# Kernel tuning notes

Measured on AMD Instinct MI355X. Metric: run time of the kernel, lower is better.

## Reference

```python
import jax, jax.numpy as jnp
import numpy as np

N_NODES = 50000
N_EDGES = 640000
HIDDEN = 128
EDGE_FEATS = 16
NUM_LAYERS = 4
NUM_GRAPHS = 64
LN_EPS = 1e-5


def setup_inputs() -> dict:
    key = jax.random.key(0)
    ks = jax.random.split(key, 12)
    s = 1.0 / np.sqrt(HIDDEN)
    se = 1.0 / np.sqrt(EDGE_FEATS)
    return {
        "x": jax.random.normal(ks[0], (N_NODES, HIDDEN), jnp.float32),
        "batch_index": jnp.sort(jax.random.randint(ks[1], (N_NODES,), 0, NUM_GRAPHS)),
        "edge_index": jax.random.randint(ks[2], (2, N_EDGES), 0, N_NODES),
        "edge_attr": jax.random.normal(ks[3], (N_EDGES, EDGE_FEATS), jnp.float32),
        # edge_transform Linear(EDGE_FEATS -> HIDDEN)
        "We": jax.random.uniform(ks[4], (EDGE_FEATS, HIDDEN), jnp.float32, -se, se),
        "be": jax.random.uniform(ks[5], (HIDDEN,), jnp.float32, -se, se),
        # per-layer GINE MLP: Linear-ReLU-Linear, stacked over layers
        "W1": jax.random.uniform(ks[6], (NUM_LAYERS, HIDDEN, HIDDEN), jnp.float32, -s, s),
        "b1": jax.random.uniform(ks[7], (NUM_LAYERS, HIDDEN), jnp.float32, -s, s),
        "W2": jax.random.uniform(ks[8], (NUM_LAYERS, HIDDEN, HIDDEN), jnp.float32, -s, s),
        "b2": jax.random.uniform(ks[9], (NUM_LAYERS, HIDDEN), jnp.float32, -s, s),
        # per-layer LayerNorm params
        "ln_g": jnp.ones((NUM_LAYERS, HIDDEN), jnp.float32),
        "ln_b": jnp.zeros((NUM_LAYERS, HIDDEN), jnp.float32),
    }


def reference(x, batch_index, edge_index, edge_attr, We, be, W1, b1, W2, b2, ln_g, ln_b):
    n = x.shape[0]
    src, dst = edge_index[0], edge_index[1]
    ea = edge_attr @ We + be  # [E, H] shared across layers
    h = x
    for l in range(W1.shape[0]):
        # GINEConv message: ReLU(x_j + edge_attr), scatter-sum at dst
        m = jax.nn.relu(h[src] + ea)
        agg = jax.ops.segment_sum(m, dst, num_segments=n)
        z = h + agg  # (1 + eps) * x + agg with eps = 0
        z = jax.nn.relu(z @ W1[l] + b1[l]) @ W2[l] + b2[l]
        # LayerNorm over feature dim
        mu = jnp.mean(z, axis=-1, keepdims=True)
        var = jnp.var(z, axis=-1, keepdims=True)
        z = (z - mu) / jnp.sqrt(var + LN_EPS) * ln_g[l] + ln_b[l]
        # dropout(p=0) is identity
        h = jax.nn.relu(z) + h
    return h
```

## Files before the change

kernel.cpp:

```cpp
#include <hip/hip_runtime.h>

#define HIDDEN 128
#define NLAYERS 4

typedef __attribute__((ext_vector_type(8))) short short8;
typedef __attribute__((ext_vector_type(4))) float f32x4;

__device__ __forceinline__ ushort f2bf(float f) {
    uint x = __builtin_bit_cast(uint, f);
    return (ushort)((x + 0x7fffu + ((x >> 16) & 1u)) >> 16);
}
__device__ __forceinline__ float bflo(uint u) {
    return __builtin_bit_cast(float, u << 16);
}
__device__ __forceinline__ float bfhi(uint u) {
    return __builtin_bit_cast(float, u & 0xffff0000u);
}


__global__ void hist_kernel(const int* __restrict__ dst, int* __restrict__ counts, int E) {
    int e = blockIdx.x * blockDim.x + threadIdx.x;
    if (e < E) atomicAdd(&counts[dst[e]], 1);
}

__global__ __launch_bounds__(1024) void scan_kernel(const int* __restrict__ counts,
                                                    int* __restrict__ offsets,
                                                    int* __restrict__ wpos, int n) {
    __shared__ int wsum[16];
    __shared__ int carry_s;
    const int t = threadIdx.x, wv = t >> 6, ln = t & 63;
    if (t == 0) carry_s = 0;
    __syncthreads();
    for (int base = 0; base < n; base += 4096) {
        const int i = base + t * 4;
        int4 c = {0, 0, 0, 0};
        if (i + 3 < n) {
            c = *(const int4*)(counts + i);
        } else {
            if (i < n)     c.x = counts[i];
            if (i + 1 < n) c.y = counts[i + 1];
            if (i + 2 < n) c.z = counts[i + 2];
            if (i + 3 < n) c.w = counts[i + 3];
        }
        const int tsum = c.x + c.y + c.z + c.w;
        int s = tsum;
#pragma unroll
        for (int off = 1; off < 64; off <<= 1) {
            int x = __shfl_up(s, off, 64);
            if (ln >= off) s += x;
        }
        if (ln == 63) wsum[wv] = s;
        __syncthreads();
        if (t < 16) {
            int x = wsum[t];
#pragma unroll
            for (int off = 1; off < 16; off <<= 1) {
                int y = __shfl_up(x, off, 16);
                if ((t & 15) >= off) x += y;
            }
            wsum[t] = x;
        }
        __syncthreads();
        const int wbase = (wv ? wsum[wv - 1] : 0) + carry_s;
        const int excl = wbase + s - tsum;
        int4 o;
        o.x = excl;
        o.y = excl + c.x;
        o.z = o.y + c.y;
        o.w = o.z + c.z;
        if (i + 3 < n) {
            *(int4*)(offsets + i) = o;
            *(int4*)(wpos + i) = o;
        } else {
            if (i < n)     { offsets[i] = o.x;     wpos[i] = o.x; }
            if (i + 1 < n) { offsets[i + 1] = o.y; wpos[i + 1] = o.y; }
            if (i + 2 < n) { offsets[i + 2] = o.z; wpos[i + 2] = o.z; }
            if (i + 3 < n) { offsets[i + 3] = o.w; wpos[i + 3] = o.w; }
        }
        __syncthreads();
        if (t == 0) carry_s += wsum[15];
        __syncthreads();
    }
    if (t == 0) offsets[n] = carry_s;
}

__global__ void fill_kernel(const int* __restrict__ src, const int* __restrict__ dst,
                            int* __restrict__ wpos, int* __restrict__ csr_src,
                            const float4* __restrict__ edge_attr,
                            ushort* __restrict__ eattr16, int E) {
    int e = blockIdx.x * blockDim.x + threadIdx.x;
    if (e < E) {
        int d = dst[e];
        int p = atomicAdd(&wpos[d], 1);
        csr_src[p] = src[e];
        ushort* op = eattr16 + (size_t)p * 16;
#pragma unroll
        for (int part = 0; part < 4; ++part) {
            float4 v = edge_attr[(size_t)e * 4 + part];
            uint2 o;
            o.x = (uint)f2bf(v.x) | ((uint)f2bf(v.y) << 16);
            o.y = (uint)f2bf(v.z) | ((uint)f2bf(v.w) << 16);
            *(uint2*)(op + part * 4) = o;
        }
    }
}

__global__ void prep_kernel(const float* __restrict__ x, ushort* __restrict__ h16p,
                            const float* __restrict__ W1, const float* __restrict__ W2,
                            ushort* __restrict__ Wt,
                            const float* __restrict__ We, const float* __restrict__ be,
                            ushort* __restrict__ WecolX, int n) {
    int i = blockIdx.x * blockDim.x + threadIdx.x;
    const int na = n * 16;
    if (i < na) {
        int row = i >> 4, lm = i & 15;
        const float* xp = x + (size_t)row * HIDDEN + lm;
        uint4 o;
        o.x = (uint)f2bf(xp[0])  | ((uint)f2bf(xp[16]) << 16);
        o.y = (uint)f2bf(xp[32]) | ((uint)f2bf(xp[48]) << 16);
        o.z = (uint)f2bf(xp[64]) | ((uint)f2bf(xp[80]) << 16);
        o.w = (uint)f2bf(xp[96]) | ((uint)f2bf(xp[112]) << 16);
        *(uint4*)(h16p + (size_t)row * HIDDEN + lm * 8) = o;
        return;
    }
    i -= na;
    if (i < NLAYERS * 2 * HIDDEN * HIDDEN) {
        int l = i >> 15;
        int m = (i >> 14) & 1;
        int nn = (i >> 7) & 127;
        int kpos = i & 127;
        int kk = (m == 0) ? (((kpos & 7) << 4) | (kpos >> 3)) : kpos;
        const float* W = m ? W2 : W1;
        Wt[i] = f2bf(W[l * 16384 + kk * 128 + nn]);
        return;
    }
    i -= NLAYERS * 2 * HIDDEN * HIDDEN;
    if (i < 128 * 32) {
        int ch = i >> 5, k = i & 31;
        float v = (k < 16) ? We[k * HIDDEN + ch] : ((k == 16) ? be[ch] : 0.f);
        WecolX[i] = f2bf(v);
    }
}

__global__ __launch_bounds__(256) void agg_kernel(const ushort* __restrict__ h16p,
                                                  const int* __restrict__ csr_src,
                                                  const ushort* __restrict__ eattr16,
                                                  const int* __restrict__ offsets,
                                                  const ushort* __restrict__ WecolX,
                                                  ushort* __restrict__ z0p, int n) {
    const int w = threadIdx.x >> 6, l = threadIdx.x & 63;
    const int lm = l & 15, lg = l >> 4;

    short8 bfr[8];
#pragma unroll
    for (int nt = 0; nt < 8; ++nt)
        bfr[nt] = *(const short8*)(WecolX + (size_t)(nt * 16 + lm) * 32 + lg * 8);

    for (int rep = 0; rep < 2; ++rep) {
        const int v = blockIdx.x * 8 + w + rep * 4;
        if (v >= n) continue;

        const int e0 = offsets[v], e1 = offsets[v + 1];
        float acc[8];
#pragma unroll
        for (int i = 0; i < 8; ++i) acc[i] = 0.f;

        for (int B = e0; B < e1; B += 16) {
            short8 af;
            if (lg < 2) {
                int ae = B + lm;
                if (ae >= e1) ae = e1 - 1;
                af = *(const short8*)(eattr16 + (size_t)ae * 16 + lg * 8);
            } else if (lg == 2) {
                af = short8{(short)0x3F80, 0, 0, 0, 0, 0, 0, 0};
            } else {
                af = short8{0, 0, 0, 0, 0, 0, 0, 0};
            }

            float vm[4];
            int sj[4];
#pragma unroll
            for (int j = 0; j < 4; ++j) {
                int e = B + lg * 4 + j;
                vm[j] = (e < e1) ? 1.f : 0.f;
                int ec = (e < e1) ? e : (e1 - 1);
                sj[j] = csr_src[ec];
            }
            uint4 hv[4];
#pragma unroll
            for (int j = 0; j < 4; ++j)
                hv[j] = *(const uint4*)(h16p + (size_t)sj[j] * HIDDEN + lm * 8);

#pragma unroll
            for (int nt = 0; nt < 8; ++nt) {
                f32x4 c = {0.f, 0.f, 0.f, 0.f};
                f32x4 d = __builtin_amdgcn_mfma_f32_16x16x32_bf16(af, bfr[nt], c, 0, 0, 0);
#pragma unroll
                for (int j = 0; j < 4; ++j) {
                    uint word = (nt < 2) ? hv[j].x : (nt < 4) ? hv[j].y
                              : (nt < 6) ? hv[j].z : hv[j].w;
                    float hc = (nt & 1) ? bfhi(word) : bflo(word);
                    acc[nt] = fmaf(vm[j], fmaxf(d[j] + hc, 0.f), acc[nt]);
                }
            }
        }

#pragma unroll
        for (int i = 0; i < 8; ++i) {
            acc[i] += __shfl_xor(acc[i], 16, 64);
            acc[i] += __shfl_xor(acc[i], 32, 64);
        }

        if (lg == 0) {
            const uint4 sv = *(const uint4*)(h16p + (size_t)v * HIDDEN + lm * 8);
            uint4 o;
            o.x = (uint)f2bf(bflo(sv.x) + acc[0]) | ((uint)f2bf(bfhi(sv.x) + acc[1]) << 16);
            o.y = (uint)f2bf(bflo(sv.y) + acc[2]) | ((uint)f2bf(bfhi(sv.y) + acc[3]) << 16);
            o.z = (uint)f2bf(bflo(sv.z) + acc[4]) | ((uint)f2bf(bfhi(sv.z) + acc[5]) << 16);
            o.w = (uint)f2bf(bflo(sv.w) + acc[6]) | ((uint)f2bf(bfhi(sv.w) + acc[7]) << 16);
            *(uint4*)(z0p + (size_t)v * HIDDEN + lm * 8) = o;
        }
    }
}

__global__ __launch_bounds__(256, 3) void mlp_kernel(const ushort* __restrict__ z0p,
                                                     ushort* __restrict__ h16p,
                                                     float* __restrict__ h32,
                                                     const ushort* __restrict__ W1t,
                                                     const ushort* __restrict__ W2t,
                                                     const float* __restrict__ b1,
                                                     const float* __restrict__ b2,
                                                     const float* __restrict__ lng,
                                                     const float* __restrict__ lnb,
                                                     int n, int last) {
    __shared__ char smem[49152];
    const int t = threadIdx.x, l = t & 63, w = t >> 6;
    const int lm = l & 15, lg = l >> 4;
    const int r0 = blockIdx.x * 64;

#pragma unroll
    for (int j = 0; j < 8; ++j) {
        int idx = t + j * 256;
        int byte = (idx * 16) ^ (((idx >> 4) & 7) << 4);
        *(short8*)(smem + byte) = *(const short8*)(W1t + idx * 8);
    }

    float b1v[8], b2v[8], lngv[8], lnbv[8];
#pragma unroll
    for (int nt = 0; nt < 8; ++nt) {
        int col = nt * 16 + lm;
        b1v[nt] = b1[col]; b2v[nt] = b2[col];
        lngv[nt] = lng[col]; lnbv[nt] = lnb[col];
    }

    short8 a[4];
    {
        int arow = r0 + w * 16 + lm;
        if (arow >= n) arow = n - 1;
        const ushort* zp = z0p + (size_t)arow * HIDDEN + lg * 8;
#pragma unroll
        for (int kk = 0; kk < 4; ++kk) a[kk] = *(const short8*)(zp + kk * 32);
    }
    __syncthreads();

    f32x4 acc[8];
#pragma unroll
    for (int nt = 0; nt < 8; ++nt) {
        f32x4 c = {0.f, 0.f, 0.f, 0.f};
#pragma unroll
        for (int kk = 0; kk < 4; ++kk) {
            int nrow = nt * 16 + lm;
            int byte = (nrow * 256 + kk * 64 + lg * 16) ^ ((nrow & 7) << 4);
            short8 b = *(const short8*)(smem + byte);
            c = __builtin_amdgcn_mfma_f32_16x16x32_bf16(a[kk], b, c, 0, 0, 0);
        }
        acc[nt] = c;
    }

#pragma unroll
    for (int nt = 0; nt < 8; ++nt) {
        int col = nt * 16 + lm;
#pragma unroll
        for (int j = 0; j < 4; ++j) {
            int rw = w * 16 + lg * 4 + j;
            int byte = (rw * 256 + col * 2) ^ ((rw & 7) << 4);
            *(ushort*)(smem + 32768 + byte) = f2bf(fmaxf(acc[nt][j] + b1v[nt], 0.f));
        }
    }
    __syncthreads();

#pragma unroll
    for (int j = 0; j < 8; ++j) {
        int idx = t + j * 256;
        int byte = (idx * 16) ^ (((idx >> 4) & 7) << 4);
        *(short8*)(smem + byte) = *(const short8*)(W2t + idx * 8);
    }
    short8 a2[4];
    {
        int rw = w * 16 + lm;
#pragma unroll
        for (int kk = 0; kk < 4; ++kk) {
            int byte = (rw * 256 + kk * 64 + lg * 16) ^ ((rw & 7) << 4);
            a2[kk] = *(const short8*)(smem + 32768 + byte);
        }
    }
    __syncthreads();

    f32x4 acc2[8];
#pragma unroll
    for (int nt = 0; nt < 8; ++nt) {
        f32x4 c = {0.f, 0.f, 0.f, 0.f};
#pragma unroll
        for (int kk = 0; kk < 4; ++kk) {
            int nrow = nt * 16 + lm;
            int byte = (nrow * 256 + kk * 64 + lg * 16) ^ ((nrow & 7) << 4);
            short8 b = *(const short8*)(smem + byte);
            c = __builtin_amdgcn_mfma_f32_16x16x32_bf16(a2[kk], b, c, 0, 0, 0);
        }
        acc2[nt] = c;
    }

    float val[8][4];
#pragma unroll
    for (int nt = 0; nt < 8; ++nt)
#pragma unroll
        for (int j = 0; j < 4; ++j) val[nt][j] = acc2[nt][j] + b2v[nt];

    float mu[4], rs[4];
#pragma unroll
    for (int j = 0; j < 4; ++j) {
        float s = 0.f;
#pragma unroll
        for (int nt = 0; nt < 8; ++nt) s += val[nt][j];
        s += __shfl_xor(s, 1, 64); s += __shfl_xor(s, 2, 64);
        s += __shfl_xor(s, 4, 64); s += __shfl_xor(s, 8, 64);
        mu[j] = s * (1.f / 128.f);
        float d2 = 0.f;
#pragma unroll
        for (int nt = 0; nt < 8; ++nt) {
            float d = val[nt][j] - mu[j];
            d2 = fmaf(d, d, d2);
        }
        d2 += __shfl_xor(d2, 1, 64); d2 += __shfl_xor(d2, 2, 64);
        d2 += __shfl_xor(d2, 4, 64); d2 += __shfl_xor(d2, 8, 64);
        rs[j] = rsqrtf(d2 * (1.f / 128.f) + 1e-5f);
    }

#pragma unroll
    for (int j = 0; j < 4; ++j) {
        int grow = r0 + w * 16 + lg * 4 + j;
        if (grow < n) {
            const uint4 hvv = *(const uint4*)(h16p + (size_t)grow * HIDDEN + lm * 8);
            float hc[8] = {bflo(hvv.x), bfhi(hvv.x), bflo(hvv.y), bfhi(hvv.y),
                           bflo(hvv.z), bfhi(hvv.z), bflo(hvv.w), bfhi(hvv.w)};
            float y[8];
#pragma unroll
            for (int nt = 0; nt < 8; ++nt)
                y[nt] = fmaxf((val[nt][j] - mu[j]) * rs[j] * lngv[nt] + lnbv[nt], 0.f) + hc[nt];
            if (last) {
#pragma unroll
                for (int nt = 0; nt < 8; ++nt)
                    h32[(size_t)grow * HIDDEN + nt * 16 + lm] = y[nt];
            } else {
                uint4 o4;
                o4.x = (uint)f2bf(y[0]) | ((uint)f2bf(y[1]) << 16);
                o4.y = (uint)f2bf(y[2]) | ((uint)f2bf(y[3]) << 16);
                o4.z = (uint)f2bf(y[4]) | ((uint)f2bf(y[5]) << 16);
                o4.w = (uint)f2bf(y[6]) | ((uint)f2bf(y[7]) << 16);
                *(uint4*)(h16p + (size_t)grow * HIDDEN + lm * 8) = o4;
            }
        }
    }
}


extern "C" void kernel_launch(void* const* d_in, const int* in_sizes, int n_in,
                              void* d_out, int out_size, void* d_ws, size_t ws_size,
                              hipStream_t stream) {
    const float* x     = (const float*)d_in[0];
    const int*   ei    = (const int*)d_in[2];
    const float* eattr = (const float*)d_in[3];
    const float* We    = (const float*)d_in[4];
    const float* be    = (const float*)d_in[5];
    const float* W1    = (const float*)d_in[6];
    const float* b1    = (const float*)d_in[7];
    const float* W2    = (const float*)d_in[8];
    const float* b2    = (const float*)d_in[9];
    const float* lng   = (const float*)d_in[10];
    const float* lnb   = (const float*)d_in[11];
    float* h32 = (float*)d_out;

    const int n = in_sizes[0] / HIDDEN;
    const int E = in_sizes[2] / 2;
    const int* src = ei;
    const int* dst = ei + E;

    size_t off = 0;
    auto take = [&](size_t bytes) {
        void* p = (char*)d_ws + off;
        off += (bytes + 255) & ~(size_t)255;
        return p;
    };
    ushort* z0p     = (ushort*)take((size_t)n * HIDDEN * 2);
    ushort* h16p    = (ushort*)take((size_t)n * HIDDEN * 2);
    ushort* Wt      = (ushort*)take((size_t)NLAYERS * 2 * HIDDEN * HIDDEN * 2);
    ushort* WecolX  = (ushort*)take((size_t)HIDDEN * 32 * 2);
    int*    counts  = (int*)take((size_t)n * 4);
    int*    offsets = (int*)take(((size_t)n + 1) * 4);
    int*    wpos    = (int*)take((size_t)n * 4);
    int*    csr_src = (int*)take((size_t)E * 4);
    ushort* eattr16 = (ushort*)take((size_t)E * 16 * 2);

    const int prep_total = n * 16 + NLAYERS * 2 * HIDDEN * HIDDEN + 128 * 32;
    prep_kernel<<<(prep_total + 255) / 256, 256, 0, stream>>>(x, h16p, W1, W2, Wt,
                                                              We, be, WecolX, n);

    hipMemsetAsync(counts, 0, (size_t)n * 4, stream);
    int eb = (E + 255) / 256;
    hist_kernel<<<eb, 256, 0, stream>>>(dst, counts, E);
    scan_kernel<<<1, 1024, 0, stream>>>(counts, offsets, wpos, n);
    fill_kernel<<<eb, 256, 0, stream>>>(src, dst, wpos, csr_src,
                                        (const float4*)eattr, eattr16, E);

    for (int lyr = 0; lyr < NLAYERS; ++lyr) {
        agg_kernel<<<(n + 7) / 8, 256, 0, stream>>>(h16p, csr_src, eattr16, offsets,
                                                    WecolX, z0p, n);
        mlp_kernel<<<(n + 63) / 64, 256, 0, stream>>>(z0p, h16p, h32,
                                                      Wt + (size_t)(lyr * 2 + 0) * 16384,
                                                      Wt + (size_t)(lyr * 2 + 1) * 16384,
                                                      b1 + (size_t)lyr * HIDDEN,
                                                      b2 + (size_t)lyr * HIDDEN,
                                                      lng + (size_t)lyr * HIDDEN,
                                                      lnb + (size_t)lyr * HIDDEN,
                                                      n, lyr == NLAYERS - 1);
    }
}
```

Measured before the change: 356.2 us.

## Prefetch next edge chunk in aggregation and use sentinel row for masking

```diff
diff --git a/kernel.cpp b/kernel.cpp
--- a/kernel.cpp
+++ b/kernel.cpp
@@ -93,15 +93,22 @@
         int d = dst[e];
         int p = atomicAdd(&wpos[d], 1);
         csr_src[p] = src[e];
+        float4 v0 = edge_attr[(size_t)e * 4 + 0];
+        float4 v1 = edge_attr[(size_t)e * 4 + 1];
+        float4 v2 = edge_attr[(size_t)e * 4 + 2];
+        float4 v3 = edge_attr[(size_t)e * 4 + 3];
+        uint4 q0, q1;
+        q0.x = (uint)f2bf(v0.x) | ((uint)f2bf(v0.y) << 16);
+        q0.y = (uint)f2bf(v0.z) | ((uint)f2bf(v0.w) << 16);
+        q0.z = (uint)f2bf(v1.x) | ((uint)f2bf(v1.y) << 16);
+        q0.w = (uint)f2bf(v1.z) | ((uint)f2bf(v1.w) << 16);
+        q1.x = (uint)f2bf(v2.x) | ((uint)f2bf(v2.y) << 16);
+        q1.y = (uint)f2bf(v2.z) | ((uint)f2bf(v2.w) << 16);
+        q1.z = (uint)f2bf(v3.x) | ((uint)f2bf(v3.y) << 16);
+        q1.w = (uint)f2bf(v3.z) | ((uint)f2bf(v3.w) << 16);
         ushort* op = eattr16 + (size_t)p * 16;
-#pragma unroll
-        for (int part = 0; part < 4; ++part) {
-            float4 v = edge_attr[(size_t)e * 4 + part];
-            uint2 o;
-            o.x = (uint)f2bf(v.x) | ((uint)f2bf(v.y) << 16);
-            o.y = (uint)f2bf(v.z) | ((uint)f2bf(v.w) << 16);
-            *(uint2*)(op + part * 4) = o;
-        }
+        *(uint4*)(op) = q0;
+        *(uint4*)(op + 8) = q1;
     }
 }
 
@@ -139,6 +146,12 @@
         int ch = i >> 5, k = i & 31;
         float v = (k < 16) ? We[k * HIDDEN + ch] : ((k == 16) ? be[ch] : 0.f);
         WecolX[i] = f2bf(v);
+        return;
+    }
+    i -= 128 * 32;
+    if (i < 16) {
+        uint4 s = {0xFF7FFF7Fu, 0xFF7FFF7Fu, 0xFF7FFF7Fu, 0xFF7FFF7Fu};
+        *(uint4*)(h16p + (size_t)n * HIDDEN + i * 8) = s;
     }
 }
 
@@ -165,43 +178,53 @@
 #pragma unroll
         for (int i = 0; i < 8; ++i) acc[i] = 0.f;
 
-        for (int B = e0; B < e1; B += 16) {
-            short8 af;
+        auto loadchunk = [&](int B, short8& af_, uint4* hv_) {
             if (lg < 2) {
                 int ae = B + lm;
                 if (ae >= e1) ae = e1 - 1;
-                af = *(const short8*)(eattr16 + (size_t)ae * 16 + lg * 8);
+                af_ = *(const short8*)(eattr16 + (size_t)ae * 16 + lg * 8);
             } else if (lg == 2) {
-                af = short8{(short)0x3F80, 0, 0, 0, 0, 0, 0, 0};
+                af_ = short8{(short)0x3F80, 0, 0, 0, 0, 0, 0, 0};
             } else {
-                af = short8{0, 0, 0, 0, 0, 0, 0, 0};
-            }
-
-            float vm[4];
-            int sj[4];
+                af_ = short8{0, 0, 0, 0, 0, 0, 0, 0};
+            }
 #pragma unroll
             for (int j = 0; j < 4; ++j) {
                 int e = B + lg * 4 + j;
-                vm[j] = (e < e1) ? 1.f : 0.f;
                 int ec = (e < e1) ? e : (e1 - 1);
-                sj[j] = csr_src[ec];
-            }
-            uint4 hv[4];
-#pragma unroll
-            for (int j = 0; j < 4; ++j)
-                hv[j] = *(const uint4*)(h16p + (size_t)sj[j] * HIDDEN + lm * 8);
+                int s = csr_src[ec];
+                s = (e < e1) ? s : n;
+                hv_[j] = *(const uint4*)(h16p + (size_t)s * HIDDEN + lm * 8);
+            }
+        };
+
+        short8 afc;
+        uint4 hvc[4];
+        if (e0 < e1) loadchunk(e0, afc, hvc);
+
+        for (int B = e0; B < e1; B += 16) {
+            short8 afn;
+            uint4 hvn[4];
+            const bool more = (B + 16) < e1;
+            if (more) loadchunk(B + 16, afn, hvn);
 
 #pragma unroll
             for (int nt = 0; nt < 8; ++nt) {
                 f32x4 c = {0.f, 0.f, 0.f, 0.f};
-                f32x4 d = __builtin_amdgcn_mfma_f32_16x16x32_bf16(af, bfr[nt], c, 0, 0, 0);
+                f32x4 d = __builtin_amdgcn_mfma_f32_16x16x32_bf16(afc, bfr[nt], c, 0, 0, 0);
 #pragma unroll
                 for (int j = 0; j < 4; ++j) {
-                    uint word = (nt < 2) ? hv[j].x : (nt < 4) ? hv[j].y
-                              : (nt < 6) ? hv[j].z : hv[j].w;
+                    uint word = (nt < 2) ? hvc[j].x : (nt < 4) ? hvc[j].y
+                              : (nt < 6) ? hvc[j].z : hvc[j].w;
                     float hc = (nt & 1) ? bfhi(word) : bflo(word);
-                    acc[nt] = fmaf(vm[j], fmaxf(d[j] + hc, 0.f), acc[nt]);
+                    acc[nt] += fmaxf(d[j] + hc, 0.f);
                 }
+            }
+
+            if (more) {
+                afc = afn;
+#pragma unroll
+                for (int j = 0; j < 4; ++j) hvc[j] = hvn[j];
             }
         }
 
@@ -402,7 +425,7 @@
         return p;
     };
     ushort* z0p     = (ushort*)take((size_t)n * HIDDEN * 2);
-    ushort* h16p    = (ushort*)take((size_t)n * HIDDEN * 2);
+    ushort* h16p    = (ushort*)take((size_t)(n + 1) * HIDDEN * 2);
     ushort* Wt      = (ushort*)take((size_t)NLAYERS * 2 * HIDDEN * HIDDEN * 2);
     ushort* WecolX  = (ushort*)take((size_t)HIDDEN * 32 * 2);
     int*    counts  = (int*)take((size_t)n * 4);
@@ -411,7 +434,7 @@
     int*    csr_src = (int*)take((size_t)E * 4);
     ushort* eattr16 = (ushort*)take((size_t)E * 16 * 2);
 
-    const int prep_total = n * 16 + NLAYERS * 2 * HIDDEN * HIDDEN + 128 * 32;
+    const int prep_total = n * 16 + NLAYERS * 2 * HIDDEN * HIDDEN + 128 * 32 + 16;
     prep_kernel<<<(prep_total + 255) / 256, 256, 0, stream>>>(x, h16p, W1, W2, Wt,
                                                               We, be, WecolX, n);
 
```

Measured after the change: 559.7 us. +57.2%, slower.
